# Kernel tuning notes

Measured on AMD Instinct MI355X. Metric: run time of the kernel, lower is better.

The kernel has to match this reference:

```python
import jax, jax.numpy as jnp
import numpy as np

B, T, H = 1, 1024, 2048
HK, HV, DK, DV, K = 8, 16, 128, 128, 4
KD = HK * DK          # 1024
VD = HV * DV          # 2048
CD = 2 * KD + VD      # conv channels: q|k|v = 4096
EPS = 1e-6


def setup_inputs() -> dict:
    key = jax.random.key(0)
    ks = jax.random.split(key, 9)
    sc = lambda k, shape, s=0.02: jax.random.normal(k, shape, jnp.float32) * s
    return {
        "x": jax.random.normal(ks[0], (B, T, H), jnp.float32),
        "w_qkvz": sc(ks[1], (H, 2 * KD + 2 * VD)),
        "w_ba": sc(ks[2], (H, 2 * HV)),
        "conv_w": sc(ks[3], (CD, K), 0.2),
        "conv_b": jnp.zeros((CD,), jnp.float32),
        "a_log": jnp.log(jax.random.uniform(ks[4], (HV,), jnp.float32, 0.5, 4.0)),
        "dt_bias": sc(ks[5], (HV,), 0.5),
        "norm_w": jnp.ones((DV,), jnp.float32),
        "w_o": sc(ks[6], (VD, H)),
    }


def _l2norm(t):
    return t * jax.lax.rsqrt(jnp.sum(t * t, axis=-1, keepdims=True) + EPS)


def _gdn_forward(x, w_qkvz, w_ba, conv_w, conv_b, a_log, dt_bias, norm_w, w_o):
    # fused qkvz projection  [B,T, 2*KD + 2*VD]
    qkvz = x @ w_qkvz
    q, k, v, z = jnp.split(qkvz, [KD, 2 * KD, 2 * KD + VD], axis=-1)
    ba = x @ w_ba
    b, a = jnp.split(ba, [HV], axis=-1)  # [B,T,HV] each

    # causal depthwise conv1d over time on concatenated q|k|v channels, then SiLU
    mixed = jnp.concatenate([q, k, v], axis=-1)          # [B,T,CD]
    xc = jnp.moveaxis(mixed, 1, 2)                       # [B,CD,T]
    xc = jnp.pad(xc, ((0, 0), (0, 0), (K - 1, 0)))       # left pad -> causal
    yc = jax.lax.conv_general_dilated(
        xc, conv_w[:, None, :], (1,), "VALID",
        dimension_numbers=("NCH", "OIH", "NCH"), feature_group_count=CD)
    yc = jax.nn.silu(yc + conv_b[None, :, None])
    mixed = jnp.moveaxis(yc, 1, 2)                       # [B,T,CD]
    q, k, v = jnp.split(mixed, [KD, 2 * KD], axis=-1)

    q = q.reshape(B, T, HK, DK)
    k = k.reshape(B, T, HK, DK)
    v = v.reshape(B, T, HV, DV)

    # qk l2 norm (use_qk_l2norm_in_kernel) + GQA repeat + scale
    q = _l2norm(q)
    k = _l2norm(k)
    groups = HV // HK
    q = jnp.repeat(q, groups, axis=2)                    # [B,T,HV,DK]
    k = jnp.repeat(k, groups, axis=2)
    q = q * (DK ** -0.5)

    beta = jax.nn.sigmoid(b)                                        # [B,T,HV]
    g = -jnp.exp(a_log)[None, None, :] * jax.nn.softplus(a + dt_bias[None, None, :])

    # gated delta rule recurrence over time
    def step(S, inp):
        qt, kt, vt, gt, bt = inp                         # [B,HV,*]
        S = S * jnp.exp(gt)[..., None, None]             # decay
        pred = jnp.einsum("bhk,bhkv->bhv", kt, S)        # retrieve
        delta = (vt - pred) * bt[..., None]              # delta update
        S = S + kt[..., None] * delta[:, :, None, :]
        o = jnp.einsum("bhk,bhkv->bhv", qt, S)
        return S, o

    S0 = jnp.zeros((B, HV, DK, DV), jnp.float32)
    xs = tuple(jnp.moveaxis(t, 1, 0) for t in (q, k, v, g, beta))
    _, o = jax.lax.scan(step, S0, xs)                    # o: [T,B,HV,DV]
    o = jnp.moveaxis(o, 0, 1)                            # [B,T,HV,DV]

    # gated RMSNorm: gate first (silu), then normalize, then scale
    zg = z.reshape(B, T, HV, DV)
    h = o * jax.nn.silu(zg)
    h = h * jax.lax.rsqrt(jnp.mean(h * h, axis=-1, keepdims=True) + EPS)
    h = h * norm_w

    return h.reshape(B, T, VD) @ w_o                     # [B,T,H]


def reference(x, w_qkvz, w_ba, conv_w, conv_b, a_log, dt_bias, norm_w, w_o):
    return _gdn_forward(x, w_qkvz, w_ba, conv_w, conv_b, a_log, dt_bias, norm_w, w_o)
```

## Files before the change

kernel.cpp:

```cpp
#include <hip/hip_runtime.h>
#include <math.h>

typedef unsigned short u16;
using us4  = __attribute__((ext_vector_type(4))) unsigned short;
using us8  = __attribute__((ext_vector_type(8))) unsigned short;
using bf16x8 = __attribute__((ext_vector_type(8))) __bf16;
using f32x4v = __attribute__((ext_vector_type(4))) float;

#define T_    1024
#define H_    2048
#define HK_   8
#define HV_   16
#define KD_   1024
#define VD_   2048
#define CD_   4096
#define QN_   6144
#define NC_   16
#define C_    64

__device__ __forceinline__ u16 f2bf(float f) {
  unsigned u = __float_as_uint(f);
  u += 0x7fffu + ((u >> 16) & 1u);
  return (u16)(u >> 16);
}
__device__ __forceinline__ float bf2f(u16 h) {
  return __uint_as_float(((unsigned)h) << 16);
}
__device__ __forceinline__ int permk3(int r, int k) {
  return (k & ~63) | ((((k >> 3) & 7) ^ (r & 7)) << 3) | (k & 7);
}

__global__ void cast_bf16(const float* __restrict__ in, u16* __restrict__ out,
                          int n8) {
  int i = blockIdx.x * 256 + threadIdx.x;
  if (i >= n8) return;
  float4 a = ((const float4*)in)[i * 2];
  float4 b = ((const float4*)in)[i * 2 + 1];
  us8 r = {f2bf(a.x), f2bf(a.y), f2bf(a.z), f2bf(a.w),
           f2bf(b.x), f2bf(b.y), f2bf(b.z), f2bf(b.w)};
  const int row = i >> 8;
  const int ip = (i & ~7) | ((i & 7) ^ (row & 7));
  *(us8*)&out[(size_t)ip * 8] = r;
}

__global__ __launch_bounds__(256) void transpose_bf16(
    const float* __restrict__ in, u16* __restrict__ out, int R, int C) {
  __shared__ float tile[64][65];
  const int r0 = blockIdx.x * 64, c0 = blockIdx.y * 64;
  const int t = threadIdx.x;
  const int tr = t >> 4, tc4 = (t & 15) * 4;
#pragma unroll
  for (int i = 0; i < 4; ++i) {
    float4 v = *(const float4*)&in[(size_t)(r0 + tr + i * 16) * C + c0 + tc4];
    tile[tr + i * 16][tc4 + 0] = v.x;
    tile[tr + i * 16][tc4 + 1] = v.y;
    tile[tr + i * 16][tc4 + 2] = v.z;
    tile[tr + i * 16][tc4 + 3] = v.w;
  }
  __syncthreads();
#pragma unroll
  for (int i = 0; i < 4; ++i) {
    int oc = tr + i * 16;
    int row = c0 + oc;
    int k = r0 + tc4;
    us4 w = {f2bf(tile[tc4 + 0][oc]), f2bf(tile[tc4 + 1][oc]),
             f2bf(tile[tc4 + 2][oc]), f2bf(tile[tc4 + 3][oc])};
    *(us4*)&out[(size_t)row * R + permk3(row, k)] = w;
  }
}

__device__ __forceinline__ void gload_lds16(const void* g, void* l) {
  __builtin_amdgcn_global_load_lds(
      (const __attribute__((address_space(1))) void*)g,
      (__attribute__((address_space(3))) void*)l, 16, 0, 0);
}

__global__ __launch_bounds__(256) void gemm_bf16(
    const u16* __restrict__ A, const u16* __restrict__ Bt,
    float* __restrict__ Cq, int ldq, float* __restrict__ Cz, int ldz,
    int zsplit, int M, int N, int K) {
  __shared__ __align__(16) u16 As[2][8192];
  __shared__ __align__(16) u16 Bs[2][4096];
  const int tid  = threadIdx.x;
  const int wave = tid >> 6, lane = tid & 63;
  const int gy = N >> 6;
  const int ncolpx = gy >> 3;
  const int bid = blockIdx.x;
  const int xcd = bid & 7, idx = bid >> 3;
  const int row0 = (idx / ncolpx) * 128;
  const int col0 = (xcd * ncolpx + idx % ncolpx) * 64;
  const int wr = wave >> 1, wc = wave & 1;
  const int fr = lane & 15, fq = lane >> 4;

  const int sr8 = lane >> 3;
  const int sc8 = (lane & 7) * 8;
  const u16* gA = A  + (size_t)(row0 + wave * 32 + sr8) * K + sc8;
  const u16* gB = Bt + (size_t)(col0 + wave * 16 + sr8) * K + sc8;

  f32x4v acc[4][2] = {};
  const int nt = K >> 6;

  auto stage = [&](int p, int k0) {
#pragma unroll
    for (int j = 0; j < 4; ++j)
      gload_lds16(gA + (size_t)(j * 8) * K + k0,
                  &As[p][(wave * 32 + j * 8) * 64]);
#pragma unroll
    for (int j = 0; j < 2; ++j)
      gload_lds16(gB + (size_t)(j * 8) * K + k0,
                  &Bs[p][(wave * 16 + j * 8) * 64]);
  };

  stage(0, 0);
  asm volatile("s_waitcnt vmcnt(0)" ::: "memory");
  __syncthreads();

  int p = 0;
  for (int it = 0; it < nt; ++it) {
    if (it + 1 < nt) stage(p ^ 1, (it + 1) * 64);
#pragma unroll
    for (int kt = 0; kt < 2; ++kt) {
      bf16x8 af[4], bff[2];
#pragma unroll
      for (int mi = 0; mi < 4; ++mi) {
        const int r = wr * 64 + mi * 16 + fr;
        af[mi] = *(const bf16x8*)
            &As[p][r * 64 + kt * 32 + (((kt * 4 + fq) ^ (r & 7)) & 3) * 8
                   + ((((kt * 4 + fq) ^ (r & 7)) >> 2) - kt) * 32];
      }
#pragma unroll
      for (int ni = 0; ni < 2; ++ni) {
        const int r = wc * 32 + ni * 16 + fr;
        bff[ni] = *(const bf16x8*)
            &Bs[p][r * 64 + kt * 32 + (((kt * 4 + fq) ^ (r & 7)) & 3) * 8
                   + ((((kt * 4 + fq) ^ (r & 7)) >> 2) - kt) * 32];
      }
#pragma unroll
      for (int mi = 0; mi < 4; ++mi)
#pragma unroll
        for (int ni = 0; ni < 2; ++ni)
          acc[mi][ni] = __builtin_amdgcn_mfma_f32_16x16x32_bf16(
              af[mi], bff[ni], acc[mi][ni], 0, 0, 0);
    }
    if (it + 1 < nt) {
      asm volatile("s_waitcnt vmcnt(0)" ::: "memory");
      __syncthreads();
    }
    p ^= 1;
  }

  float* Cp; int ldc, cb;
  if (col0 < zsplit) { Cp = Cq; ldc = ldq; cb = col0; }
  else               { Cp = Cz; ldc = ldz; cb = col0 - zsplit; }
#pragma unroll
  for (int mi = 0; mi < 4; ++mi)
#pragma unroll
    for (int ni = 0; ni < 2; ++ni) {
      const int r  = row0 + wr * 64 + mi * 16 + fq * 4;
      const int cc = cb + wc * 32 + ni * 16 + fr;
#pragma unroll
      for (int j = 0; j < 4; ++j)
        Cp[(size_t)(r + j) * ldc + cc] = acc[mi][ni][j];
    }
}

__global__ __launch_bounds__(256) void ba_gbeta(
    const float* __restrict__ x, const float* __restrict__ w_ba,
    const float* __restrict__ a_log, const float* __restrict__ dt_bias,
    float* __restrict__ g, float* __restrict__ beta) {
  const int t = blockIdx.x;
  const int tid = threadIdx.x;
  __shared__ float xs[2048];
  __shared__ float red[8][32];
  {
    float4 v = *(const float4*)&x[(size_t)t * H_ + tid * 4];
    *(float4*)&xs[tid * 4] = v;
    float4 w = *(const float4*)&x[(size_t)t * H_ + 1024 + tid * 4];
    *(float4*)&xs[1024 + tid * 4] = w;
  }
  __syncthreads();
  const int c = tid & 31;
  const int chunk = tid >> 5;
  float p = 0.f;
  const int kb = chunk * 256;
#pragma unroll 4
  for (int k = kb; k < kb + 256; ++k) p = fmaf(xs[k], w_ba[k * 32 + c], p);
  red[chunk][c] = p;
  __syncthreads();
  if (tid < 32) {
    float s = 0.f;
#pragma unroll
    for (int i = 0; i < 8; ++i) s += red[i][c];
    if (c < 16) {
      beta[t * 16 + c] = 1.f / (1.f + expf(-s));
    } else {
      int h = c - 16;
      float xx = s + dt_bias[h];
      float sp = xx > 20.f ? xx : log1pf(expf(xx));
      g[t * 16 + h] = -expf(a_log[h]) * sp;
    }
  }
}

__global__ __launch_bounds__(512) void conv_silu_k(
    const float* __restrict__ qkvraw, const float* __restrict__ conv_w,
    const float* __restrict__ conv_b, float* __restrict__ qkvc,
    float* __restrict__ khat) {
  const int t = blockIdx.x;
  const int tid = threadIdx.x;
  const int c0 = tid * 8;
  float acc[8];
  float4 cb0 = *(const float4*)&conv_b[c0];
  float4 cb1 = *(const float4*)&conv_b[c0 + 4];
  acc[0] = cb0.x; acc[1] = cb0.y; acc[2] = cb0.z; acc[3] = cb0.w;
  acc[4] = cb1.x; acc[5] = cb1.y; acc[6] = cb1.z; acc[7] = cb1.w;
  float wv[8][4];
#pragma unroll
  for (int i = 0; i < 8; i += 2) {
    float4 w0 = *(const float4*)&conv_w[(c0 + i) * 4];
    float4 w1 = *(const float4*)&conv_w[(c0 + i + 1) * 4];
    wv[i][0] = w0.x; wv[i][1] = w0.y; wv[i][2] = w0.z; wv[i][3] = w0.w;
    wv[i+1][0] = w1.x; wv[i+1][1] = w1.y; wv[i+1][2] = w1.z; wv[i+1][3] = w1.w;
  }
#pragma unroll
  for (int j = 0; j < 4; ++j) {
    int tt = t - 3 + j;
    if (tt >= 0) {
      float4 a = *(const float4*)&qkvraw[(size_t)tt * CD_ + c0];
      float4 b = *(const float4*)&qkvraw[(size_t)tt * CD_ + c0 + 4];
      float xv[8] = {a.x, a.y, a.z, a.w, b.x, b.y, b.z, b.w};
#pragma unroll
      for (int i = 0; i < 8; ++i) acc[i] = fmaf(xv[i], wv[i][j], acc[i]);
    }
  }
  float y[8];
#pragma unroll
  for (int i = 0; i < 8; ++i) y[i] = acc[i] / (1.f + expf(-acc[i]));

  if (tid < 128 || tid >= 256) {
    float4 o0 = {y[0], y[1], y[2], y[3]};
    float4 o1 = {y[4], y[5], y[6], y[7]};
    *(float4*)&qkvc[(size_t)t * CD_ + c0]     = o0;
    *(float4*)&qkvc[(size_t)t * CD_ + c0 + 4] = o1;
  } else {
    float ss = 0.f;
#pragma unroll
    for (int i = 0; i < 8; ++i) ss = fmaf(y[i], y[i], ss);
#pragma unroll
    for (int off = 1; off < 16; off <<= 1) ss += __shfl_xor(ss, off);
    float rs = rsqrtf(ss + 1e-6f);
    const int head = (c0 - 1024) >> 7;
    const int d0 = (c0 - 1024) & 127;
    float4 o0 = {y[0] * rs, y[1] * rs, y[2] * rs, y[3] * rs};
    float4 o1 = {y[4] * rs, y[5] * rs, y[6] * rs, y[7] * rs};
    float* kout = &khat[((size_t)t * HK_ + head) * 128 + d0];
    *(float4*)&kout[0] = o0;
    *(float4*)&kout[4] = o1;
  }
}

#define SWZ(r) (((r) >> 2) & 7)

__device__ __forceinline__ float4 ldsw4(const float* base, int r, int dblk) {
  return *(const float4*)&base[r * 128 + ((dblk ^ SWZ(r)) << 2)];
}
__device__ __forceinline__ float ldsw1(const float* base, int r, int d) {
  return base[r * 128 + ((((d) >> 2) ^ SWZ(r)) << 2) + ((d) & 3)];
}

__global__ __launch_bounds__(256) void chunk_prep(
    const float* __restrict__ qkvc, const float* __restrict__ khat,
    const float* __restrict__ g, const float* __restrict__ beta,
    float* __restrict__ cgbuf, float* __restrict__ Wtg, float* __restrict__ Ug,
    float* __restrict__ Mqg, float* __restrict__ pQg) {
  const int c = blockIdx.x, hv = blockIdx.y, hk = hv >> 1;
  const int cid = c * 16 + hv;
  const int tid = threadIdx.x;
  __shared__ float Kl[8192], Ql[8192];
  __shared__ float AM[8320];
  __shared__ float cgl[64], bl[64], bp[64], rsl[64];
  float* At = AM;
  float* Mq = AM + 4160;

#pragma unroll
  for (int it = 0; it < 8; ++it) {
    int flat = it * 1024 + tid * 4;
    int row = flat >> 7, d = flat & 127;
    int pb = ((d >> 2) ^ SWZ(row)) << 2;
    int gt = c * 64 + row;
    float4 kv = *(const float4*)&khat[((size_t)gt * HK_ + hk) * 128 + d];
    float4 qv = *(const float4*)&qkvc[(size_t)gt * CD_ + hk * 128 + d];
    *(float4*)&Kl[row * 128 + pb] = kv;
    *(float4*)&Ql[row * 128 + pb] = qv;
  }
  if (tid < 64) {
    float s = g[(size_t)(c * 64 + tid) * HV_ + hv];
#pragma unroll
    for (int off = 1; off < 64; off <<= 1) {
      float t = __shfl_up(s, off);
      if (tid >= off) s += t;
    }
    cgl[tid] = s;
    cgbuf[cid * 64 + tid] = s;
    bl[tid] = beta[(size_t)(c * 64 + tid) * HV_ + hv];
  }
  __syncthreads();
  if (tid < 64) {
    float sq = 0.f;
#pragma unroll
    for (int dblk = 0; dblk < 32; ++dblk) {
      float4 q4 = ldsw4(Ql, tid, dblk);
      sq = fmaf(q4.x, q4.x, sq); sq = fmaf(q4.y, q4.y, sq);
      sq = fmaf(q4.z, q4.z, sq); sq = fmaf(q4.w, q4.w, sq);
    }
    rsl[tid] = rsqrtf(sq + 1e-6f) * 0.08838834764831845f;
    bp[tid] = bl[tid] * expf(cgl[tid]);
  }
  __syncthreads();

  const int i0 = (tid >> 4) * 4, j0 = (tid & 15) * 4;
  float kk[4][4], qk[4][4];
#pragma unroll
  for (int a = 0; a < 4; ++a)
#pragma unroll
    for (int b = 0; b < 4; ++b) { kk[a][b] = 0.f; qk[a][b] = 0.f; }
  for (int dblk = 0; dblk < 32; ++dblk) {
    float4 ka[4], qa[4], kb[4];
#pragma unroll
    for (int a = 0; a < 4; ++a) {
      ka[a] = ldsw4(Kl, i0 + a, dblk);
      qa[a] = ldsw4(Ql, i0 + a, dblk);
    }
#pragma unroll
    for (int b = 0; b < 4; ++b) kb[b] = ldsw4(Kl, j0 + b, dblk);
#pragma unroll
    for (int a = 0; a < 4; ++a)
#pragma unroll
      for (int b = 0; b < 4; ++b) {
        kk[a][b] = fmaf(ka[a].x, kb[b].x, kk[a][b]);
        kk[a][b] = fmaf(ka[a].y, kb[b].y, kk[a][b]);
        kk[a][b] = fmaf(ka[a].z, kb[b].z, kk[a][b]);
        kk[a][b] = fmaf(ka[a].w, kb[b].w, kk[a][b]);
        qk[a][b] = fmaf(qa[a].x, kb[b].x, qk[a][b]);
        qk[a][b] = fmaf(qa[a].y, kb[b].y, qk[a][b]);
        qk[a][b] = fmaf(qa[a].z, kb[b].z, qk[a][b]);
        qk[a][b] = fmaf(qa[a].w, kb[b].w, qk[a][b]);
      }
  }
#pragma unroll
  for (int a = 0; a < 4; ++a)
#pragma unroll
    for (int b = 0; b < 4; ++b) {
      int i = i0 + a, j = j0 + b;
      float e = expf(cgl[i] - cgl[j]);
      At[j * 65 + i] = (j < i) ? (-bl[i] * e * kk[a][b]) : 0.f;
      Mq[j * 65 + i] = (j <= i) ? (rsl[i] * e * qk[a][b]) : 0.f;
    }
  __syncthreads();

  float X[64];
  if (tid < 128) {
#pragma unroll
    for (int j = 0; j < 64; ++j) X[j] = bp[j] * ldsw1(Kl, j, tid);
  } else {
    const int m = tid - 128;
#pragma unroll
    for (int j = 0; j < 64; ++j)
      X[j] = bl[j] * qkvc[(size_t)(c * 64 + j) * CD_ + 2 * KD_ + hv * 128 + m];
  }
#pragma unroll
  for (int it = 0; it < 16; ++it) {
    int f = it * 256 + tid;
    int j = f >> 6, i = f & 63;
    Mqg[(size_t)cid * 4096 + f] = Mq[j * 65 + i];
  }
#pragma unroll
  for (int j = 0; j < 63; ++j) {
    float xj = X[j];
#pragma unroll
    for (int i = j + 1; i < 64; ++i) X[i] = fmaf(At[j * 65 + i], xj, X[i]);
  }
  __syncthreads();

  if (tid < 128) {
    size_t baseo = ((size_t)cid * 128 + tid) * 64;
#pragma unroll
    for (int j4 = 0; j4 < 16; ++j4) {
      float4 v = {X[j4 * 4], X[j4 * 4 + 1], X[j4 * 4 + 2], X[j4 * 4 + 3]};
      *(float4*)&Wtg[baseo + j4 * 4] = v;
    }
  } else {
    const int m = tid - 128;
    float* Utr = AM;
#pragma unroll
    for (int j = 0; j < 64; ++j) Utr[j * 128 + m] = X[j];
  }
  __syncthreads();
  {
    const float* Utr = AM;
#pragma unroll
    for (int it = 0; it < 8; ++it) {
      int flat = it * 1024 + tid * 4;
      *(float4*)&Ug[(size_t)cid * 8192 + flat] = *(const float4*)&Utr[flat];
    }
    const int i = tid & 63;
    const float ei = expf(cgl[i]) * rsl[i];
#pragma unroll
    for (int it = 0; it < 32; ++it) {
      int d = it * 4 + (tid >> 6);
      pQg[(size_t)cid * 8192 + d * 64 + i] = ei * ldsw1(Ql, i, d);
    }
  }
}

__global__ __launch_bounds__(256) void make_MBG(
    const float* __restrict__ Wtg, const float* __restrict__ pQg,
    const float* __restrict__ Ug, const float* __restrict__ Mqg,
    const float* __restrict__ khat, const float* __restrict__ cgbuf,
    u16* __restrict__ Mhi, u16* __restrict__ Mlo,
    float* __restrict__ Bg, float* __restrict__ Gtg) {
  const int c = blockIdx.x, hv = blockIdx.y, hk = hv >> 1;
  const int cid = c * 16 + hv;
  const int tid = threadIdx.x;
  __shared__ float Wl[64 * 128];
  __shared__ float Kel[64 * 128];
  __shared__ float Ul[64 * 128];
  __shared__ float Mql[64 * 64];
  const float cg63 = cgbuf[cid * 64 + 63];
  const float pC = expf(cg63);
#pragma unroll
  for (int it = 0; it < 8; ++it) {
    int f = it * 1024 + tid * 4;
    int d = f >> 6, j = f & 63;
    float4 w = *(const float4*)&Wtg[(size_t)cid * 8192 + f];
    Wl[(j + 0) * 128 + d] = w.x;
    Wl[(j + 1) * 128 + d] = w.y;
    Wl[(j + 2) * 128 + d] = w.z;
    Wl[(j + 3) * 128 + d] = w.w;
  }
#pragma unroll
  for (int it = 0; it < 8; ++it) {
    int f = it * 1024 + tid * 4;
    int j = f >> 7, d = f & 127;
    float esc = expf(cg63 - cgbuf[cid * 64 + j]);
    float4 kv = *(const float4*)&khat[((size_t)(c * 64 + j) * HK_ + hk) * 128 + d];
    float4 uv = *(const float4*)&Ug[(size_t)cid * 8192 + f];
    kv.x *= esc; kv.y *= esc; kv.z *= esc; kv.w *= esc;
    *(float4*)&Kel[f] = kv;
    *(float4*)&Ul[f] = uv;
  }
#pragma unroll
  for (int it = 0; it < 4; ++it) {
    int f = it * 1024 + tid * 4;
    *(float4*)&Mql[f] = *(const float4*)&Mqg[(size_t)cid * 4096 + f];
  }
  __syncthreads();

  const int d0 = (tid & 15) * 8, n0 = (tid >> 4) * 8;
  float ma[8][8] = {}, ba[8][8] = {};
  for (int j = 0; j < 64; ++j) {
    float4 k0 = *(const float4*)&Kel[j * 128 + d0];
    float4 k1 = *(const float4*)&Kel[j * 128 + d0 + 4];
    float4 w0 = *(const float4*)&Wl[j * 128 + n0];
    float4 w1 = *(const float4*)&Wl[j * 128 + n0 + 4];
    float4 u0 = *(const float4*)&Ul[j * 128 + n0];
    float4 u1 = *(const float4*)&Ul[j * 128 + n0 + 4];
    float ke[8] = {k0.x, k0.y, k0.z, k0.w, k1.x, k1.y, k1.z, k1.w};
    float wv[8] = {w0.x, w0.y, w0.z, w0.w, w1.x, w1.y, w1.z, w1.w};
    float uv[8] = {u0.x, u0.y, u0.z, u0.w, u1.x, u1.y, u1.z, u1.w};
#pragma unroll
    for (int a = 0; a < 8; ++a)
#pragma unroll
      for (int b = 0; b < 8; ++b) {
        ma[a][b] = fmaf(ke[a], wv[b], ma[a][b]);
        ba[a][b] = fmaf(ke[a], uv[b], ba[a][b]);
      }
  }
#pragma unroll
  for (int a = 0; a < 8; ++a) {
    const int d = d0 + a;
    us8 hi, lo;
#pragma unroll
    for (int b = 0; b < 8; ++b) {
      float m = ((d == n0 + b) ? pC : 0.f) - ma[a][b];
      u16 h = f2bf(m);
      hi[b] = h;
      lo[b] = f2bf(m - bf2f(h));
    }
    *(us8*)&Mhi[(size_t)cid * 16384 + d * 128 + n0] = hi;
    *(us8*)&Mlo[(size_t)cid * 16384 + d * 128 + n0] = lo;
    float4 b0 = {ba[a][0], ba[a][1], ba[a][2], ba[a][3]};
    float4 b1 = {ba[a][4], ba[a][5], ba[a][6], ba[a][7]};
    *(float4*)&Bg[(size_t)cid * 16384 + d * 128 + n0]     = b0;
    *(float4*)&Bg[(size_t)cid * 16384 + d * 128 + n0 + 4] = b1;
  }

  const int dg = (tid & 31) * 4, ig = (tid >> 5) * 8;
  float ga[4][8] = {};
  for (int j = 0; j < 64; ++j) {
    float4 w4 = *(const float4*)&Wl[j * 128 + dg];
    float4 m0 = *(const float4*)&Mql[j * 64 + ig];
    float4 m1 = *(const float4*)&Mql[j * 64 + ig + 4];
    float wv[4] = {w4.x, w4.y, w4.z, w4.w};
    float mv[8] = {m0.x, m0.y, m0.z, m0.w, m1.x, m1.y, m1.z, m1.w};
#pragma unroll
    for (int a = 0; a < 4; ++a)
#pragma unroll
      for (int b = 0; b < 8; ++b) ga[a][b] = fmaf(wv[a], mv[b], ga[a][b]);
  }
#pragma unroll
  for (int a = 0; a < 4; ++a) {
    const int d = dg + a;
    float4 p0 = *(const float4*)&pQg[(size_t)cid * 8192 + d * 64 + ig];
    float4 p1 = *(const float4*)&pQg[(size_t)cid * 8192 + d * 64 + ig + 4];
    float4 g0 = {p0.x - ga[a][0], p0.y - ga[a][1], p0.z - ga[a][2], p0.w - ga[a][3]};
    float4 g1 = {p1.x - ga[a][4], p1.y - ga[a][5], p1.z - ga[a][6], p1.w - ga[a][7]};
    *(float4*)&Gtg[(size_t)cid * 8192 + d * 64 + ig]     = g0;
    *(float4*)&Gtg[(size_t)cid * 8192 + d * 64 + ig + 4] = g1;
  }
}

__global__ __launch_bounds__(512) void scan_S(
    const u16* __restrict__ Mhi, const u16* __restrict__ Mlo,
    const float* __restrict__ Bg, float* __restrict__ Sg) {
  const int flat = blockIdx.x;
  const int hv = (flat & 7) + 8 * (flat >> 5);
  const int vs = (flat >> 3) & 3;
  const int tid = threadIdx.x;
  const int wave = tid >> 6, lane = tid & 63;
  const int fr = lane & 15, fq = lane >> 4;
  const int wr = wave * 16;
  const int m0 = vs * 32;

  __shared__ u16 Sh[2][4096];
  __shared__ u16 Sl[2][4096];

  for (int i = tid; i < 4096; i += 512) { Sh[0][i] = 0; Sl[0][i] = 0; }
  {
    float* s0 = Sg + (size_t)hv * 16384 + m0;
#pragma unroll
    for (int it = 0; it < 8; ++it) {
      int idx = it * 512 + tid;
      s0[(size_t)(idx >> 5) * 128 + (idx & 31)] = 0.f;
    }
  }
  __syncthreads();

  bf16x8 MhA[4], MlA[4], MhB[4], MlB[4];
  {
    const u16* Mh0 = Mhi + (size_t)hv * 16384;
    const u16* Ml0 = Mlo + (size_t)hv * 16384;
#pragma unroll
    for (int kt = 0; kt < 4; ++kt) {
      size_t off = (size_t)(wr + fr) * 128 + kt * 32 + fq * 8;
      MhA[kt] = *(const bf16x8*)&Mh0[off];
      MlA[kt] = *(const bf16x8*)&Ml0[off];
    }
  }
  int p = 0;

  auto step = [&](int c, bf16x8 (&MhC)[4], bf16x8 (&MlC)[4],
                  bf16x8 (&MhN)[4], bf16x8 (&MlN)[4]) {
    if (c + 1 < NC_ - 1) {
      const u16* MhP = Mhi + (size_t)((c + 1) * 16 + hv) * 16384;
      const u16* MlP = Mlo + (size_t)((c + 1) * 16 + hv) * 16384;
#pragma unroll
      for (int kt = 0; kt < 4; ++kt) {
        size_t off = (size_t)(wr + fr) * 128 + kt * 32 + fq * 8;
        MhN[kt] = *(const bf16x8*)&MhP[off];
        MlN[kt] = *(const bf16x8*)&MlP[off];
      }
    }
    const float* Bc = Bg + (size_t)(c * 16 + hv) * 16384 + m0;
    float bv[2][4];
#pragma unroll
    for (int b = 0; b < 2; ++b)
#pragma unroll
      for (int j = 0; j < 4; ++j)
        bv[b][j] = Bc[(size_t)(wr + fq * 4 + j) * 128 + b * 16 + fr];

    f32x4v acc[2] = {};
#pragma unroll
    for (int kt = 0; kt < 4; ++kt) {
      bf16x8 Bh[2], Bl[2];
#pragma unroll
      for (int b = 0; b < 2; ++b) {
        int m = b * 16 + fr;
        int byte = m * 256 + ((kt * 64 + fq * 16) ^ ((m & 7) << 4));
        Bh[b] = *(const bf16x8*)((const char*)&Sh[p][0] + byte);
        Bl[b] = *(const bf16x8*)((const char*)&Sl[p][0] + byte);
      }
#pragma unroll
      for (int b = 0; b < 2; ++b) {
        acc[b] = __builtin_amdgcn_mfma_f32_16x16x32_bf16(
            MlC[kt], Bh[b], acc[b], 0, 0, 0);
        acc[b] = __builtin_amdgcn_mfma_f32_16x16x32_bf16(
            MhC[kt], Bl[b], acc[b], 0, 0, 0);
        acc[b] = __builtin_amdgcn_mfma_f32_16x16x32_bf16(
            MhC[kt], Bh[b], acc[b], 0, 0, 0);
      }
    }
    float* Sn = Sg + (size_t)((c + 1) * 16 + hv) * 16384 + m0;
#pragma unroll
    for (int b = 0; b < 2; ++b) {
      const int k0 = wr + fq * 4;
      const int m = b * 16 + fr;
      us4 h4, l4;
#pragma unroll
      for (int j = 0; j < 4; ++j) {
        float v = acc[b][j] + bv[b][j];
        Sn[(size_t)(k0 + j) * 128 + m] = v;
        u16 h = f2bf(v);
        h4[j] = h;
        l4[j] = f2bf(v - bf2f(h));
      }
      int byte = m * 256 + (((k0 * 2)) ^ ((m & 7) << 4));
      *(us4*)((char*)&Sh[p ^ 1][0] + byte) = h4;
      *(us4*)((char*)&Sl[p ^ 1][0] + byte) = l4;
    }
    __syncthreads();
    p ^= 1;
  };

  for (int cc = 0; cc < NC_ - 1; cc += 2) {
    step(cc, MhA, MlA, MhB, MlB);
    if (cc + 1 < NC_ - 1) step(cc + 1, MhB, MlB, MhA, MlA);
  }
}

__global__ __launch_bounds__(256) void chunk_out(
    const float* __restrict__ Mqg, const float* __restrict__ Ug,
    const float* __restrict__ Gtg, const float* __restrict__ Sg,
    float* __restrict__ o) {
  const int c = blockIdx.x, hv = blockIdx.y;
  const int cid = c * 16 + hv;
  const int tid = threadIdx.x;
  __shared__ float Mql[64 * 64];
  __shared__ float Ul[64 * 128];
  __shared__ float Gtl[128 * 64];
  __shared__ float Sl[128 * 128];
#pragma unroll
  for (int it = 0; it < 4; ++it) {
    int f = it * 1024 + tid * 4;
    *(float4*)&Mql[f] = *(const float4*)&Mqg[(size_t)cid * 4096 + f];
  }
#pragma unroll
  for (int it = 0; it < 8; ++it) {
    int f = it * 1024 + tid * 4;
    *(float4*)&Ul[f]  = *(const float4*)&Ug[(size_t)cid * 8192 + f];
    *(float4*)&Gtl[f] = *(const float4*)&Gtg[(size_t)cid * 8192 + f];
  }
#pragma unroll
  for (int it = 0; it < 16; ++it) {
    int f = it * 1024 + tid * 4;
    *(float4*)&Sl[f] = *(const float4*)&Sg[(size_t)cid * 16384 + f];
  }
  __syncthreads();

  const int i0 = (tid & 15) * 4, m0 = (tid >> 4) * 8;
  float oa[4][8] = {};
  for (int j = 0; j < 64; ++j) {
    float4 mq = *(const float4*)&Mql[j * 64 + i0];
    float4 u0 = *(const float4*)&Ul[j * 128 + m0];
    float4 u1 = *(const float4*)&Ul[j * 128 + m0 + 4];
    float mv[4] = {mq.x, mq.y, mq.z, mq.w};
    float uv[8] = {u0.x, u0.y, u0.z, u0.w, u1.x, u1.y, u1.z, u1.w};
#pragma unroll
    for (int a = 0; a < 4; ++a)
#pragma unroll
      for (int b = 0; b < 8; ++b) oa[a][b] = fmaf(mv[a], uv[b], oa[a][b]);
  }
  for (int d = 0; d < 128; ++d) {
    float4 gt = *(const float4*)&Gtl[d * 64 + i0];
    float4 s0 = *(const float4*)&Sl[d * 128 + m0];
    float4 s1 = *(const float4*)&Sl[d * 128 + m0 + 4];
    float gv[4] = {gt.x, gt.y, gt.z, gt.w};
    float sv[8] = {s0.x, s0.y, s0.z, s0.w, s1.x, s1.y, s1.z, s1.w};
#pragma unroll
    for (int a = 0; a < 4; ++a)
#pragma unroll
      for (int b = 0; b < 8; ++b) oa[a][b] = fmaf(gv[a], sv[b], oa[a][b]);
  }
#pragma unroll
  for (int a = 0; a < 4; ++a) {
    const int t = c * 64 + i0 + a;
    float4 o0 = {oa[a][0], oa[a][1], oa[a][2], oa[a][3]};
    float4 o1 = {oa[a][4], oa[a][5], oa[a][6], oa[a][7]};
    *(float4*)&o[((size_t)t * HV_ + hv) * 128 + m0]     = o0;
    *(float4*)&o[((size_t)t * HV_ + hv) * 128 + m0 + 4] = o1;
  }
}

__global__ void gated_rmsnorm(const float* __restrict__ o,
                              const float* __restrict__ zbuf,
                              const float* __restrict__ norm_w,
                              u16* __restrict__ h) {
  const int t = blockIdx.x, hv = blockIdx.y, d = threadIdx.x;
  float ov = o[((size_t)t * HV_ + hv) * 128 + d];
  float zv = zbuf[(size_t)t * VD_ + hv * 128 + d];
  float hc = ov * (zv / (1.f + expf(-zv)));
  float ss = hc * hc;
#pragma unroll
  for (int off = 32; off >= 1; off >>= 1) ss += __shfl_xor(ss, off);
  __shared__ float s2[2];
  if ((d & 63) == 0) s2[d >> 6] = ss;
  __syncthreads();
  float tot = s2[0] + s2[1];
  float r = rsqrtf(tot * (1.f / 128.f) + 1e-6f);
  const int k = hv * 128 + d;
  h[(size_t)t * VD_ + permk3(t, k)] = f2bf(hc * r * norm_w[d]);
}

extern "C" void kernel_launch(void* const* d_in, const int* in_sizes, int n_in,
                              void* d_out, int out_size, void* d_ws, size_t ws_size,
                              hipStream_t stream) {
  const float* x       = (const float*)d_in[0];
  const float* w_qkvz  = (const float*)d_in[1];
  const float* w_ba    = (const float*)d_in[2];
  const float* conv_w  = (const float*)d_in[3];
  const float* conv_b  = (const float*)d_in[4];
  const float* a_log   = (const float*)d_in[5];
  const float* dt_bias = (const float*)d_in[6];
  const float* norm_w  = (const float*)d_in[7];
  const float* w_o     = (const float*)d_in[8];
  float* out = (float*)d_out;

  float* ws = (float*)d_ws;
  float* qkvraw = ws;
  float* zbuf   = ws + 4194304;
  float* qkvc   = ws + 6291456;
  float* khat   = ws + 10485760;
  float* gbuf   = ws + 11534336;
  float* bbuf   = ws + 11550720;
  float* cgbuf  = ws + 11567104;
  float* obuf   = ws + 11583488;
  float* Wtg    = ws + 13680640;
  float* pQg    = ws + 15777792;
  float* Ug     = ws + 17874944;
  float* Mqg    = ws + 19972096;
  float* Gtg    = ws + 21020672;

  u16* xb   = (u16*)obuf;
  u16* wqt  = (u16*)Wtg;
  u16* Mhi  = (u16*)qkvc;
  u16* Mlo  = (u16*)(qkvc + 2097152);
  float* Bg = qkvraw;
  float* Sg = Wtg;
  u16* wot  = (u16*)qkvc;
  u16* hb   = (u16*)khat;

  cast_bf16<<<1024, 256, 0, stream>>>(x, xb, 262144);
  transpose_bf16<<<dim3(32, 96), 256, 0, stream>>>(w_qkvz, wqt, H_, QN_);
  gemm_bf16<<<768, 256, 0, stream>>>(xb, wqt, qkvraw, CD_, zbuf, VD_,
                                     CD_, T_, QN_, H_);
  ba_gbeta<<<T_, 256, 0, stream>>>(x, w_ba, a_log, dt_bias, gbuf, bbuf);
  conv_silu_k<<<T_, 512, 0, stream>>>(qkvraw, conv_w, conv_b, qkvc, khat);
  chunk_prep<<<dim3(NC_, HV_), 256, 0, stream>>>(
      qkvc, khat, gbuf, bbuf, cgbuf, Wtg, Ug, Mqg, pQg);
  make_MBG<<<dim3(NC_, HV_), 256, 0, stream>>>(
      Wtg, pQg, Ug, Mqg, khat, cgbuf, Mhi, Mlo, Bg, Gtg);
  scan_S<<<64, 512, 0, stream>>>(Mhi, Mlo, Bg, Sg);
  transpose_bf16<<<dim3(32, 32), 256, 0, stream>>>(w_o, wot, VD_, H_);
  chunk_out<<<dim3(NC_, HV_), 256, 0, stream>>>(Mqg, Ug, Gtg, Sg, obuf);
  gated_rmsnorm<<<dim3(T_, HV_), 128, 0, stream>>>(obuf, zbuf, norm_w, hb);
  gemm_bf16<<<256, 256, 0, stream>>>(hb, wot, out, VD_, out, VD_,
                                     VD_, T_, VD_, H_);
}
```

Before: 259.7 us.

## Double block size of chunk_prep and make_MBG to 512 threads with warp-specialized stores

Both per-chunk preparation kernels now launch 512 threads instead of 256, halving the per-thread register tile in the GEMM-like loops. In chunk_prep the extra 256 threads take over the Mqg and pQg output writes while the first 256 run the triangular solve, so those stores overlap the serial forward substitution. Only 256 blocks exist, so the aim is more waves per CU to hide latency in these launch-limited kernels. The cost is smaller per-thread tiles, which lowers LDS data reuse, and a larger block that may be limited by LDS or register occupancy.

```diff
diff --git a/kernel.cpp b/kernel.cpp
--- a/kernel.cpp
+++ b/kernel.cpp
@@ -268,7 +268,7 @@
   return base[r * 128 + ((((d) >> 2) ^ SWZ(r)) << 2) + ((d) & 3)];
 }
 
-__global__ __launch_bounds__(256) void chunk_prep(
+__global__ __launch_bounds__(512) void chunk_prep(
     const float* __restrict__ qkvc, const float* __restrict__ khat,
     const float* __restrict__ g, const float* __restrict__ beta,
     float* __restrict__ cgbuf, float* __restrict__ Wtg, float* __restrict__ Ug,
@@ -283,8 +283,8 @@
   float* Mq = AM + 4160;
 
 #pragma unroll
-  for (int it = 0; it < 8; ++it) {
-    int flat = it * 1024 + tid * 4;
+  for (int it = 0; it < 4; ++it) {
+    int flat = it * 2048 + tid * 4;
     int row = flat >> 7, d = flat & 127;
     int pb = ((d >> 2) ^ SWZ(row)) << 2;
     int gt = c * 64 + row;
@@ -318,25 +318,25 @@
   }
   __syncthreads();
 
-  const int i0 = (tid >> 4) * 4, j0 = (tid & 15) * 4;
-  float kk[4][4], qk[4][4];
+  const int i0 = (tid >> 5) * 4, j0 = (tid & 31) * 2;
+  float kk[4][2], qk[4][2];
 #pragma unroll
   for (int a = 0; a < 4; ++a)
 #pragma unroll
-    for (int b = 0; b < 4; ++b) { kk[a][b] = 0.f; qk[a][b] = 0.f; }
+    for (int b = 0; b < 2; ++b) { kk[a][b] = 0.f; qk[a][b] = 0.f; }
   for (int dblk = 0; dblk < 32; ++dblk) {
-    float4 ka[4], qa[4], kb[4];
+    float4 ka[4], qa[4], kb[2];
 #pragma unroll
     for (int a = 0; a < 4; ++a) {
       ka[a] = ldsw4(Kl, i0 + a, dblk);
       qa[a] = ldsw4(Ql, i0 + a, dblk);
     }
 #pragma unroll
-    for (int b = 0; b < 4; ++b) kb[b] = ldsw4(Kl, j0 + b, dblk);
+    for (int b = 0; b < 2; ++b) kb[b] = ldsw4(Kl, j0 + b, dblk);
 #pragma unroll
     for (int a = 0; a < 4; ++a)
 #pragma unroll
-      for (int b = 0; b < 4; ++b) {
+      for (int b = 0; b < 2; ++b) {
         kk[a][b] = fmaf(ka[a].x, kb[b].x, kk[a][b]);
         kk[a][b] = fmaf(ka[a].y, kb[b].y, kk[a][b]);
         kk[a][b] = fmaf(ka[a].z, kb[b].z, kk[a][b]);
@@ -350,7 +350,7 @@
 #pragma unroll
   for (int a = 0; a < 4; ++a)
 #pragma unroll
-    for (int b = 0; b < 4; ++b) {
+    for (int b = 0; b < 2; ++b) {
       int i = i0 + a, j = j0 + b;
       float e = expf(cgl[i] - cgl[j]);
       At[j * 65 + i] = (j < i) ? (-bl[i] * e * kk[a][b]) : 0.f;
@@ -359,37 +359,49 @@
   __syncthreads();
 
   float X[64];
-  if (tid < 128) {
-#pragma unroll
-    for (int j = 0; j < 64; ++j) X[j] = bp[j] * ldsw1(Kl, j, tid);
+  if (tid < 256) {
+    if (tid < 128) {
+#pragma unroll
+      for (int j = 0; j < 64; ++j) X[j] = bp[j] * ldsw1(Kl, j, tid);
+    } else {
+      const int m = tid - 128;
+#pragma unroll
+      for (int j = 0; j < 64; ++j)
+        X[j] = bl[j] * qkvc[(size_t)(c * 64 + j) * CD_ + 2 * KD_ + hv * 128 + m];
+    }
+#pragma unroll
+    for (int j = 0; j < 63; ++j) {
+      float xj = X[j];
+#pragma unroll
+      for (int i = j + 1; i < 64; ++i) X[i] = fmaf(At[j * 65 + i], xj, X[i]);
+    }
+    if (tid < 128) {
+      size_t baseo = ((size_t)cid * 128 + tid) * 64;
+#pragma unroll
+      for (int j4 = 0; j4 < 16; ++j4) {
+        float4 v = {X[j4 * 4], X[j4 * 4 + 1], X[j4 * 4 + 2], X[j4 * 4 + 3]};
+        *(float4*)&Wtg[baseo + j4 * 4] = v;
+      }
+    }
   } else {
-    const int m = tid - 128;
-#pragma unroll
-    for (int j = 0; j < 64; ++j)
-      X[j] = bl[j] * qkvc[(size_t)(c * 64 + j) * CD_ + 2 * KD_ + hv * 128 + m];
-  }
-#pragma unroll
-  for (int it = 0; it < 16; ++it) {
-    int f = it * 256 + tid;
-    int j = f >> 6, i = f & 63;
-    Mqg[(size_t)cid * 4096 + f] = Mq[j * 65 + i];
-  }
-#pragma unroll
-  for (int j = 0; j < 63; ++j) {
-    float xj = X[j];
-#pragma unroll
-    for (int i = j + 1; i < 64; ++i) X[i] = fmaf(At[j * 65 + i], xj, X[i]);
-  }
-  __syncthreads();
-
-  if (tid < 128) {
-    size_t baseo = ((size_t)cid * 128 + tid) * 64;
-#pragma unroll
-    for (int j4 = 0; j4 < 16; ++j4) {
-      float4 v = {X[j4 * 4], X[j4 * 4 + 1], X[j4 * 4 + 2], X[j4 * 4 + 3]};
-      *(float4*)&Wtg[baseo + j4 * 4] = v;
-    }
-  } else {
+    const int t2 = tid - 256;
+#pragma unroll
+    for (int it = 0; it < 16; ++it) {
+      int f = it * 256 + t2;
+      int j = f >> 6, i = f & 63;
+      Mqg[(size_t)cid * 4096 + f] = Mq[j * 65 + i];
+    }
+    const int i = t2 & 63;
+    const float ei = expf(cgl[i]) * rsl[i];
+#pragma unroll
+    for (int it = 0; it < 32; ++it) {
+      int d = it * 4 + (t2 >> 6);
+      pQg[(size_t)cid * 8192 + d * 64 + i] = ei * ldsw1(Ql, i, d);
+    }
+  }
+  __syncthreads();
+
+  if (tid >= 128 && tid < 256) {
     const int m = tid - 128;
     float* Utr = AM;
 #pragma unroll
@@ -399,21 +411,14 @@
   {
     const float* Utr = AM;
 #pragma unroll
-    for (int it = 0; it < 8; ++it) {
-      int flat = it * 1024 + tid * 4;
+    for (int it = 0; it < 4; ++it) {
+      int flat = it * 2048 + tid * 4;
       *(float4*)&Ug[(size_t)cid * 8192 + flat] = *(const float4*)&Utr[flat];
     }
-    const int i = tid & 63;
-    const float ei = expf(cgl[i]) * rsl[i];
-#pragma unroll
-    for (int it = 0; it < 32; ++it) {
-      int d = it * 4 + (tid >> 6);
-      pQg[(size_t)cid * 8192 + d * 64 + i] = ei * ldsw1(Ql, i, d);
-    }
-  }
-}
-
-__global__ __launch_bounds__(256) void make_MBG(
+  }
+}
+
+__global__ __launch_bounds__(512) void make_MBG(
     const float* __restrict__ Wtg, const float* __restrict__ pQg,
     const float* __restrict__ Ug, const float* __restrict__ Mqg,
     const float* __restrict__ khat, const float* __restrict__ cgbuf,
@@ -429,8 +434,8 @@
   const float cg63 = cgbuf[cid * 64 + 63];
   const float pC = expf(cg63);
 #pragma unroll
-  for (int it = 0; it < 8; ++it) {
-    int f = it * 1024 + tid * 4;
+  for (int it = 0; it < 4; ++it) {
+    int f = it * 2048 + tid * 4;
     int d = f >> 6, j = f & 63;
     float4 w = *(const float4*)&Wtg[(size_t)cid * 8192 + f];
     Wl[(j + 0) * 128 + d] = w.x;
@@ -439,8 +444,8 @@
     Wl[(j + 3) * 128 + d] = w.w;
   }
 #pragma unroll
-  for (int it = 0; it < 8; ++it) {
-    int f = it * 1024 + tid * 4;
+  for (int it = 0; it < 4; ++it) {
+    int f = it * 2048 + tid * 4;
     int j = f >> 7, d = f & 127;
     float esc = expf(cg63 - cgbuf[cid * 64 + j]);
     float4 kv = *(const float4*)&khat[((size_t)(c * 64 + j) * HK_ + hk) * 128 + d];
@@ -450,28 +455,26 @@
     *(float4*)&Ul[f] = uv;
   }
 #pragma unroll
-  for (int it = 0; it < 4; ++it) {
-    int f = it * 1024 + tid * 4;
+  for (int it = 0; it < 2; ++it) {
+    int f = it * 2048 + tid * 4;
     *(float4*)&Mql[f] = *(const float4*)&Mqg[(size_t)cid * 4096 + f];
   }
   __syncthreads();
 
-  const int d0 = (tid & 15) * 8, n0 = (tid >> 4) * 8;
-  float ma[8][8] = {}, ba[8][8] = {};
+  const int d0 = (tid & 15) * 8, n0 = (tid >> 4) * 4;
+  float ma[8][4] = {}, ba[8][4] = {};
   for (int j = 0; j < 64; ++j) {
     float4 k0 = *(const float4*)&Kel[j * 128 + d0];
     float4 k1 = *(const float4*)&Kel[j * 128 + d0 + 4];
     float4 w0 = *(const float4*)&Wl[j * 128 + n0];
-    float4 w1 = *(const float4*)&Wl[j * 128 + n0 + 4];
     float4 u0 = *(const float4*)&Ul[j * 128 + n0];
-    float4 u1 = *(const float4*)&Ul[j * 128 + n0 + 4];
     float ke[8] = {k0.x, k0.y, k0.z, k0.w, k1.x, k1.y, k1.z, k1.w};
-    float wv[8] = {w0.x, w0.y, w0.z, w0.w, w1.x, w1.y, w1.z, w1.w};
-    float uv[8] = {u0.x, u0.y, u0.z, u0.w, u1.x, u1.y, u1.z, u1.w};
+    float wv[4] = {w0.x, w0.y, w0.z, w0.w};
+    float uv[4] = {u0.x, u0.y, u0.z, u0.w};
 #pragma unroll
     for (int a = 0; a < 8; ++a)
 #pragma unroll
-      for (int b = 0; b < 8; ++b) {
+      for (int b = 0; b < 4; ++b) {
         ma[a][b] = fmaf(ke[a], wv[b], ma[a][b]);
         ba[a][b] = fmaf(ke[a], uv[b], ba[a][b]);
       }
@@ -479,44 +482,38 @@
 #pragma unroll
   for (int a = 0; a < 8; ++a) {
     const int d = d0 + a;
-    us8 hi, lo;
-#pragma unroll
-    for (int b = 0; b < 8; ++b) {
+    us4 hi, lo;
+#pragma unroll
+    for (int b = 0; b < 4; ++b) {
       float m = ((d == n0 + b) ? pC : 0.f) - ma[a][b];
       u16 h = f2bf(m);
       hi[b] = h;
       lo[b] = f2bf(m - bf2f(h));
     }
-    *(us8*)&Mhi[(size_t)cid * 16384 + d * 128 + n0] = hi;
-    *(us8*)&Mlo[(size_t)cid * 16384 + d * 128 + n0] = lo;
+    *(us4*)&Mhi[(size_t)cid * 16384 + d * 128 + n0] = hi;
+    *(us4*)&Mlo[(size_t)cid * 16384 + d * 128 + n0] = lo;
     float4 b0 = {ba[a][0], ba[a][1], ba[a][2], ba[a][3]};
-    float4 b1 = {ba[a][4], ba[a][5], ba[a][6], ba[a][7]};
-    *(float4*)&Bg[(size_t)cid * 16384 + d * 128 + n0]     = b0;
-    *(float4*)&Bg[(size_t)cid * 16384 + d * 128 + n0 + 4] = b1;
-  }
-
-  const int dg = (tid & 31) * 4, ig = (tid >> 5) * 8;
-  float ga[4][8] = {};
+    *(float4*)&Bg[(size_t)cid * 16384 + d * 128 + n0] = b0;
+  }
+
+  const int dg = (tid & 31) * 4, ig = (tid >> 5) * 4;
+  float ga[4][4] = {};
   for (int j = 0; j < 64; ++j) {
     float4 w4 = *(const float4*)&Wl[j * 128 + dg];
     float4 m0 = *(const float4*)&Mql[j * 64 + ig];
-    float4 m1 = *(const float4*)&Mql[j * 64 + ig + 4];
     float wv[4] = {w4.x, w4.y, w4.z, w4.w};
-    float mv[8] = {m0.x, m0.y, m0.z, m0.w, m1.x, m1.y, m1.z, m1.w};
+    float mv[4] = {m0.x, m0.y, m0.z, m0.w};
 #pragma unroll
     for (int a = 0; a < 4; ++a)
 #pragma unroll
-      for (int b = 0; b < 8; ++b) ga[a][b] = fmaf(wv[a], mv[b], ga[a][b]);
+      for (int b = 0; b < 4; ++b) ga[a][b] = fmaf(wv[a], mv[b], ga[a][b]);
   }
 #pragma unroll
   for (int a = 0; a < 4; ++a) {
     const int d = dg + a;
     float4 p0 = *(const float4*)&pQg[(size_t)cid * 8192 + d * 64 + ig];
-    float4 p1 = *(const float4*)&pQg[(size_t)cid * 8192 + d * 64 + ig + 4];
     float4 g0 = {p0.x - ga[a][0], p0.y - ga[a][1], p0.z - ga[a][2], p0.w - ga[a][3]};
-    float4 g1 = {p1.x - ga[a][4], p1.y - ga[a][5], p1.z - ga[a][6], p1.w - ga[a][7]};
-    *(float4*)&Gtg[(size_t)cid * 8192 + d * 64 + ig]     = g0;
-    *(float4*)&Gtg[(size_t)cid * 8192 + d * 64 + ig + 4] = g1;
+    *(float4*)&Gtg[(size_t)cid * 8192 + d * 64 + ig] = g0;
   }
 }
 
@@ -755,9 +752,9 @@
                                      CD_, T_, QN_, H_);
   ba_gbeta<<<T_, 256, 0, stream>>>(x, w_ba, a_log, dt_bias, gbuf, bbuf);
   conv_silu_k<<<T_, 512, 0, stream>>>(qkvraw, conv_w, conv_b, qkvc, khat);
-  chunk_prep<<<dim3(NC_, HV_), 256, 0, stream>>>(
+  chunk_prep<<<dim3(NC_, HV_), 512, 0, stream>>>(
       qkvc, khat, gbuf, bbuf, cgbuf, Wtg, Ug, Mqg, pQg);
-  make_MBG<<<dim3(NC_, HV_), 256, 0, stream>>>(
+  make_MBG<<<dim3(NC_, HV_), 512, 0, stream>>>(
       Wtg, pQg, Ug, Mqg, khat, cgbuf, Mhi, Mlo, Bg, Gtg);
   scan_S<<<64, 512, 0, stream>>>(Mhi, Mlo, Bg, Sg);
   transpose_bf16<<<dim3(32, 32), 256, 0, stream>>>(w_o, wot, VD_, H_);
```

New measurement: 250.9 us. 1.04x faster.
